# Optimization experiments

Measured on AMD Instinct MI355X. Metric: run time of the kernel, lower is better.

Reference implementation:

```python
import jax, jax.numpy as jnp
import numpy as np

N = 50000   # nodes
E = 800000  # edges
D = 200     # h_dim == out_dim
R = 500     # num_rels
L = 2       # num_hidden_layers
RRELU_SLOPE = (1.0 / 8.0 + 1.0 / 3.0) / 2.0  # eval-mode F.rrelu negative slope


def _rrelu(x):
    return jnp.where(x >= 0, x, x * jnp.float32(RRELU_SLOPE))


def setup_inputs() -> dict:
    key = jax.random.key(0)
    ks = jax.random.split(key, 10)
    s = np.float32(1.0 / np.sqrt(D))  # ~xavier scale
    return {
        "init_ent_emb": jax.random.normal(ks[0], (N, D), jnp.float32),
        "rel_emb": jax.random.normal(ks[1], (R, D), jnp.float32),
        "weight_neighbor": jax.random.normal(ks[2], (L, D, D), jnp.float32) * s,
        "loop_weight": jax.random.normal(ks[3], (L, D, D), jnp.float32) * s,
        "evolve_loop_weight": jax.random.normal(ks[4], (L, D, D), jnp.float32) * s,
        "norm": jax.random.uniform(ks[5], (N, 1), jnp.float32),
        "src": jax.random.randint(ks[6], (E,), 0, N, dtype=jnp.int32),
        "dst": jax.random.randint(ks[7], (E,), 0, N, dtype=jnp.int32),
        "etype": jax.random.randint(ks[8], (E,), 0, R, dtype=jnp.int32),
        "node_id": jnp.arange(N, dtype=jnp.int32),
    }


def reference(init_ent_emb, rel_emb, weight_neighbor, loop_weight,
              evolve_loop_weight, norm, src, dst, etype, node_id):
    # g.ndata['h'] = init_ent_emb[node_id]
    h = init_ent_emb[node_id]                                    # [N, D]
    # mask of nodes with in-degree > 0 (fixed across layers)
    indeg = jnp.zeros((N,), jnp.float32).at[dst].add(1.0)
    has_in = (indeg > 0)[:, None]                                # [N, 1]
    for l in range(L):
        # loop message: loop_weight where in-degree>0, evolve_loop_weight otherwise
        loop_msg = jnp.where(has_in,
                             h @ loop_weight[l],
                             h @ evolve_loop_weight[l])          # [N, D]
        # per-edge message: (h_src + rel_emb[etype]) @ W_neighbor
        msg = (h[src] + rel_emb[etype]) @ weight_neighbor[l]     # [E, D]
        # sum-scatter to destination nodes, then per-node norm (apply_func)
        agg = jax.ops.segment_sum(msg, dst, num_segments=N)      # [N, D]
        h = _rrelu(agg * norm + loop_msg)
    return h
```

## Files before the change

### kernel.cpp

```cpp
#include <hip/hip_runtime.h>

#define D 200
#define RRELU_SLOPE 0.22916666666666666f
#define STRIDE 96
#define PAD 8

typedef unsigned short u16;
typedef unsigned int u32;

using bf16x8 = __attribute__((ext_vector_type(8))) short;
using f32x4  = __attribute__((ext_vector_type(4))) float;
using f32x2  = __attribute__((ext_vector_type(2))) float;

__device__ __forceinline__ float rrelu(float x) {
    return x >= 0.0f ? x : x * RRELU_SLOPE;
}
__device__ __forceinline__ float bf2f(u32 u) {
    union { u32 i; float f; } c; c.i = u << 16; return c.f;
}
__device__ __forceinline__ u32 f2bf(float f) {
    union { float f; u32 i; } c; c.f = f;
    return (c.i + 0x7fffu + ((c.i >> 16) & 1u)) >> 16;
}
__device__ __forceinline__ u32 pack2(float x, float y) {
    return f2bf(x) | (f2bf(y) << 16);
}
__device__ __forceinline__ void gll16(const void* g, void* l) {
    __builtin_amdgcn_global_load_lds((const __attribute__((address_space(1))) void*)g,
                                     (__attribute__((address_space(3))) void*)l,
                                     16, 0, 0);
}

__device__ __forceinline__ void accw(u32 w, f32x2& acc) {
    union { u32 i; float f; } lo, hi;
    lo.i = w << 16;
    hi.i = w & 0xffff0000u;
    f32x2 t; t[0] = lo.f; t[1] = hi.f;
    acc += t;
}
__device__ __forceinline__ void accq(uint4 q, f32x2* a) {
    accw(q.x, a[0]); accw(q.y, a[1]); accw(q.z, a[2]); accw(q.w, a[3]);
}


__global__ void prep_k(const float* __restrict__ rel, const float* __restrict__ Wn,
                       const float* __restrict__ Wl, u16* __restrict__ relb,
                       u16* __restrict__ Bt, u16* __restrict__ hb0d,
                       u16* __restrict__ hb1d, int* __restrict__ noin_cnt) {
    int i = blockIdx.x * blockDim.x + threadIdx.x;
    if (i == 0) *noin_cnt = 0;
    if (i < 200) { hb0d[i] = 0; hb1d[i] = 0; }
    if (i < 100200) relb[i] = (i < 100000) ? (u16)f2bf(rel[i]) : (u16)0;
    if (i < 2 * 256 * 416) {
        int l = i / (256 * 416);
        int rem = i % (256 * 416);
        int c = rem / 416;
        int k = rem % 416;
        float v = 0.0f;
        if (c < 200 && k < 400)
            v = (k < 200) ? Wn[(size_t)l * 40000 + k * 200 + c]
                          : Wl[(size_t)l * 40000 + (k - 200) * 200 + c];
        Bt[i] = (u16)f2bf(v);
    }
}


__global__ void scatter_k(const int* __restrict__ dst, const int* __restrict__ src,
                          const int* __restrict__ etype, int* __restrict__ cnt,
                          u32* __restrict__ ep, int E) {
    int e = blockIdx.x * blockDim.x + threadIdx.x;
    if (e < E) {
        int d = dst[e];
        int c = atomicAdd(&cnt[d], 1);
        if (c < STRIDE)
            ep[(size_t)d * STRIDE + c] = (u32)src[e] | ((u32)etype[e] << 17);
    }
}

__global__ void pad_k(const int* __restrict__ cnt, u32* __restrict__ ep, u32 dummy,
                      int* __restrict__ noin, int* __restrict__ noin_cnt, int N) {
    int v = blockIdx.x * blockDim.x + threadIdx.x;
    if (v >= N) return;
    int c = cnt[v];
    if (c == 0) noin[atomicAdd(noin_cnt, 1)] = v;
    int e = (c + PAD - 1) & ~(PAD - 1);
    for (int i = c; i < e; ++i) ep[(size_t)v * STRIDE + i] = dummy;
}


__global__ void gather_k(const float* __restrict__ init, const int* __restrict__ nid,
                         u16* __restrict__ hb, int N) {
    int lane = threadIdx.x & 63;
    int v = blockIdx.x * 4 + (threadIdx.x >> 6);
    if (v >= N || lane >= 50) return;
    float4 f = *(const float4*)(init + (size_t)nid[v] * D + lane * 4);
    uint2 o;
    o.x = pack2(f.x, f.y);
    o.y = pack2(f.z, f.w);
    *(uint2*)(hb + (size_t)v * D + lane * 4) = o;
}


__global__ __launch_bounds__(256) void gagg0_k(
        const u16* __restrict__ hb, const u16* __restrict__ relb,
        const u32* __restrict__ ep, const int* __restrict__ cnt,
        const float* __restrict__ norm,
        u16* __restrict__ aggb, u16* __restrict__ relsumb, int N, u32 dummy) {
    int lane = threadIdx.x & 63;
    int wave = threadIdx.x >> 6;
    int li = lane & 31;
    int v = blockIdx.x * 8 + wave * 2 + (lane >> 5);
    if (v >= N || li >= 25) return;
    size_t lo = (size_t)li * 8;
    const u16* hbL = hb + lo;
    const u16* rbL = relb + lo;
    int c = cnt[v];
    if (c > STRIDE) c = STRIDE;
    int rv = (c + PAD - 1) >> 3;
    const u32* pp = ep + (size_t)v * STRIDE;
    f32x2 a[4] = {}, rr[4] = {};
    u32 p[8];
    uint4 qh[8];
#pragma unroll
    for (int j = 0; j < 8; ++j) p[j] = (rv > 0) ? pp[j] : dummy;
#pragma unroll
    for (int j = 0; j < 8; ++j)
        qh[j] = *(const uint4*)(hbL + (size_t)(p[j] & 0x1FFFFu) * D);
    for (int r = 0; r < rv; ++r) {
        u32 pn[8];
#pragma unroll
        for (int j = 0; j < 8; ++j)
            pn[j] = (r + 1 < rv) ? pp[(size_t)(r + 1) * 8 + j] : dummy;
        uint4 qr[8];
#pragma unroll
        for (int j = 0; j < 8; ++j)
            qr[j] = *(const uint4*)(rbL + (size_t)((p[j] >> 17) & 0x3FFu) * D);
#pragma unroll
        for (int j = 0; j < 8; ++j) accq(qh[j], a);
#pragma unroll
        for (int j = 0; j < 8; ++j)
            qh[j] = *(const uint4*)(hbL + (size_t)(pn[j] & 0x1FFFFu) * D);
#pragma unroll
        for (int j = 0; j < 8; ++j) accq(qr[j], rr);
#pragma unroll
        for (int j = 0; j < 8; ++j) p[j] = pn[j];
    }
    uint4 rs;
    rs.x = pack2(rr[0][0], rr[0][1]); rs.y = pack2(rr[1][0], rr[1][1]);
    rs.z = pack2(rr[2][0], rr[2][1]); rs.w = pack2(rr[3][0], rr[3][1]);
    *(uint4*)(relsumb + (size_t)v * D + lo) = rs;
    float nv = norm[v];
    uint4 o;
    o.x = pack2((a[0][0] + rr[0][0]) * nv, (a[0][1] + rr[0][1]) * nv);
    o.y = pack2((a[1][0] + rr[1][0]) * nv, (a[1][1] + rr[1][1]) * nv);
    o.z = pack2((a[2][0] + rr[2][0]) * nv, (a[2][1] + rr[2][1]) * nv);
    o.w = pack2((a[3][0] + rr[3][0]) * nv, (a[3][1] + rr[3][1]) * nv);
    *(uint4*)(aggb + (size_t)v * D + lo) = o;
}


__global__ __launch_bounds__(256) void gagg1_k(
        const u16* __restrict__ hb, const u32* __restrict__ ep,
        const int* __restrict__ cnt, const float* __restrict__ norm,
        const u16* __restrict__ addb, u16* __restrict__ outb, int N, u32 dummy) {
    int lane = threadIdx.x & 63;
    int wave = threadIdx.x >> 6;
    int li = lane & 31;
    int v = blockIdx.x * 8 + wave * 2 + (lane >> 5);
    if (v >= N || li >= 25) return;
    size_t lo = (size_t)li * 8;
    const u16* hbL = hb + lo;
    int c = cnt[v];
    if (c > STRIDE) c = STRIDE;
    int rv = (c + PAD - 1) >> 3;
    const u32* pp = ep + (size_t)v * STRIDE;
    f32x2 a[4] = {};
    u32 p[8];
    uint4 qh[8];
#pragma unroll
    for (int j = 0; j < 8; ++j) p[j] = (rv > 0) ? pp[j] : dummy;
#pragma unroll
    for (int j = 0; j < 8; ++j)
        qh[j] = *(const uint4*)(hbL + (size_t)(p[j] & 0x1FFFFu) * D);
    for (int r = 0; r < rv; ++r) {
        u32 pn[8];
#pragma unroll
        for (int j = 0; j < 8; ++j)
            pn[j] = (r + 1 < rv) ? pp[(size_t)(r + 1) * 8 + j] : dummy;
#pragma unroll
        for (int j = 0; j < 8; ++j) accq(qh[j], a);
#pragma unroll
        for (int j = 0; j < 8; ++j)
            qh[j] = *(const uint4*)(hbL + (size_t)(pn[j] & 0x1FFFFu) * D);
#pragma unroll
        for (int j = 0; j < 8; ++j) p[j] = pn[j];
    }
    {
        uint4 q = *(const uint4*)(addb + (size_t)v * D + lo);
        accq(q, a);
    }
    float nv = norm[v];
    uint4 o;
    o.x = pack2(a[0][0] * nv, a[0][1] * nv);
    o.y = pack2(a[1][0] * nv, a[1][1] * nv);
    o.z = pack2(a[2][0] * nv, a[2][1] * nv);
    o.w = pack2(a[3][0] * nv, a[3][1] * nv);
    *(uint4*)(outb + (size_t)v * D + lo) = o;
}


__global__ __launch_bounds__(256) void gemm_k(
        const u16* __restrict__ Aagg, const u16* __restrict__ Ah,
        const u16* __restrict__ Bt,
        float* __restrict__ outF, u16* __restrict__ outB, int M) {
    __shared__ __align__(16) u16 As[128 * 32];
    __shared__ __align__(16) u16 Bs[64 * 32];
    int tid = threadIdx.x;
    int lane = tid & 63;
    int wave = tid >> 6;
    int rowBase = blockIdx.x * 128;
    int colBase = blockIdx.y * 64;
    int wr = (wave >> 1) * 64;
    int wc = (wave & 1) * 32;
    int m = lane & 15;
    int kq = (lane >> 4) * 8;

    int srow = tid >> 2;
    int kg = (tid & 3) * 8;

    u16* ldsA0 = As + ((size_t)(wave * 64) * 8);
    u16* ldsA1 = As + ((size_t)(256 + wave * 64) * 8);
    u16* ldsB  = Bs + ((size_t)(wave * 64) * 8);

    f32x4 acc[4][2] = {};

    for (int k0 = 0; k0 < 416; k0 += 32) {
        int k = k0 + kg;
        {
            const u16* g0 = (k < 200) ? Aagg + (size_t)(rowBase + srow) * D + k
                                      : Ah + (size_t)(rowBase + srow) * D + (k - 200);
            gll16(g0, ldsA0);
            const u16* g1 = (k < 200) ? Aagg + (size_t)(rowBase + srow + 64) * D + k
                                      : Ah + (size_t)(rowBase + srow + 64) * D + (k - 200);
            gll16(g1, ldsA1);
            const u16* gb = Bt + (size_t)(colBase + srow) * 416 + k;
            gll16(gb, ldsB);
        }
        __syncthreads();

        bf16x8 a0 = *(const bf16x8*)(As + (wr + m) * 32 + kq);
        bf16x8 a1 = *(const bf16x8*)(As + (wr + 16 + m) * 32 + kq);
        bf16x8 a2 = *(const bf16x8*)(As + (wr + 32 + m) * 32 + kq);
        bf16x8 a3 = *(const bf16x8*)(As + (wr + 48 + m) * 32 + kq);
        bf16x8 b0 = *(const bf16x8*)(Bs + (wc + m) * 32 + kq);
        bf16x8 b1 = *(const bf16x8*)(Bs + (wc + 16 + m) * 32 + kq);
        acc[0][0] = __builtin_amdgcn_mfma_f32_16x16x32_bf16(a0, b0, acc[0][0], 0, 0, 0);
        acc[0][1] = __builtin_amdgcn_mfma_f32_16x16x32_bf16(a0, b1, acc[0][1], 0, 0, 0);
        acc[1][0] = __builtin_amdgcn_mfma_f32_16x16x32_bf16(a1, b0, acc[1][0], 0, 0, 0);
        acc[1][1] = __builtin_amdgcn_mfma_f32_16x16x32_bf16(a1, b1, acc[1][1], 0, 0, 0);
        acc[2][0] = __builtin_amdgcn_mfma_f32_16x16x32_bf16(a2, b0, acc[2][0], 0, 0, 0);
        acc[2][1] = __builtin_amdgcn_mfma_f32_16x16x32_bf16(a2, b1, acc[2][1], 0, 0, 0);
        acc[3][0] = __builtin_amdgcn_mfma_f32_16x16x32_bf16(a3, b0, acc[3][0], 0, 0, 0);
        acc[3][1] = __builtin_amdgcn_mfma_f32_16x16x32_bf16(a3, b1, acc[3][1], 0, 0, 0);
        __syncthreads();
    }

    int cRow = (lane >> 4) * 4;
    int cCol = lane & 15;
#pragma unroll
    for (int i = 0; i < 4; ++i) {
#pragma unroll
        for (int j = 0; j < 2; ++j) {
            int col = colBase + wc + j * 16 + cCol;
            if (col >= 200) continue;
#pragma unroll
            for (int r = 0; r < 4; ++r) {
                int row = rowBase + wr + i * 16 + cRow + r;
                if (row < M) {
                    float val = rrelu(acc[i][j][r]);
                    if (outF) outF[(size_t)row * D + col] = val;
                    if (outB) outB[(size_t)row * D + col] = (u16)f2bf(val);
                }
            }
        }
    }
}


__global__ void fixup_k(const u16* __restrict__ hb, const float* __restrict__ We,
                        const int* __restrict__ noin, const int* __restrict__ noin_cnt,
                        float* __restrict__ outF, u16* __restrict__ outB) {
    int cnt = *noin_cnt;
    for (int i = blockIdx.x; i < cnt; i += gridDim.x) {
        int v = noin[i];
        int j = threadIdx.x;
        if (j < D) {
            float acc = 0.0f;
            for (int k = 0; k < D; ++k)
                acc += bf2f(hb[(size_t)v * D + k]) * We[(size_t)k * D + j];
            float r = rrelu(acc);
            if (outF) outF[(size_t)v * D + j] = r;
            if (outB) outB[(size_t)v * D + j] = (u16)f2bf(r);
        }
    }
}

extern "C" void kernel_launch(void* const* d_in, const int* in_sizes, int n_in,
                              void* d_out, int out_size, void* d_ws, size_t ws_size,
                              hipStream_t stream) {
    const float* init  = (const float*)d_in[0];
    const float* rel   = (const float*)d_in[1];
    const float* Wn    = (const float*)d_in[2];
    const float* Wl    = (const float*)d_in[3];
    const float* We    = (const float*)d_in[4];
    const float* norm  = (const float*)d_in[5];
    const int* src     = (const int*)d_in[6];
    const int* dst     = (const int*)d_in[7];
    const int* etype   = (const int*)d_in[8];
    const int* node_id = (const int*)d_in[9];
    float* out = (float*)d_out;

    int N = in_sizes[5];
    int E = in_sizes[6];
    size_t NP = (size_t)N + 256;

    char* w = (char*)d_ws;
    auto carve = [&](size_t bytes) {
        char* p = w;
        w += (bytes + 255) & ~(size_t)255;
        return p;
    };
    u16* hb0     = (u16*)carve(NP * D * sizeof(u16));
    u16* hb1     = (u16*)carve(NP * D * sizeof(u16));
    u16* aggb    = (u16*)carve(NP * D * sizeof(u16));
    u16* relsumb = (u16*)carve((size_t)N * D * sizeof(u16));
    u16* relb    = (u16*)carve((size_t)501 * D * sizeof(u16));
    u16* Bt      = (u16*)carve((size_t)2 * 256 * 416 * sizeof(u16));
    int* cnt     = (int*)carve((size_t)N * sizeof(int));
    u32* epack   = (u32*)carve(((size_t)N * STRIDE + PAD) * sizeof(u32));
    int* noin    = (int*)carve((size_t)N * sizeof(int));
    int* noin_cnt = (int*)carve(sizeof(int));

    (void)hipMemsetAsync(cnt, 0, (size_t)N * sizeof(int), stream);

    int prepN = 2 * 256 * 416;
    prep_k<<<(prepN + 255) / 256, 256, 0, stream>>>(rel, Wn, Wl, relb, Bt,
                                                    hb0 + (size_t)N * D,
                                                    hb1 + (size_t)N * D, noin_cnt);
    scatter_k<<<(E + 255) / 256, 256, 0, stream>>>(dst, src, etype, cnt, epack, E);
    u32 dummy = (u32)N | (500u << 17);
    pad_k<<<(N + 255) / 256, 256, 0, stream>>>(cnt, epack, dummy, noin, noin_cnt, N);
    gather_k<<<(N + 3) / 4, 256, 0, stream>>>(init, node_id, hb0, N);

    dim3 gg((N + 127) / 128, 4);

    gagg0_k<<<(N + 7) / 8, 256, 0, stream>>>(hb0, relb, epack, cnt, norm,
                                             aggb, relsumb, N, dummy);
    gemm_k<<<gg, 256, 0, stream>>>(aggb, hb0, Bt, nullptr, hb1, N);
    fixup_k<<<8, 256, 0, stream>>>(hb0, We, noin, noin_cnt, nullptr, hb1);

    gagg1_k<<<(N + 7) / 8, 256, 0, stream>>>(hb1, epack, cnt, norm,
                                             relsumb, aggb, N, dummy);
    gemm_k<<<gg, 256, 0, stream>>>(aggb, hb1, Bt + 256 * 416, out, nullptr, N);
    fixup_k<<<8, 256, 0, stream>>>(hb1, We + D * D, noin, noin_cnt, out, nullptr);
}
```

Measured before the change: 376.5 us.

## Retile GEMM to 64-row blocks covering all output columns per block

The fused aggregation+loop GEMM now assigns each block 64 rows and all 256 padded output columns, with each wave computing a 64x64 tile, instead of a 128x64 tile over a 2D grid. The A rows (agg and h) are then read from global memory once instead of once per column block, which cuts redundant activation traffic. In exchange each block loads the full weight slice every k-step, needs more LDS and twice the accumulator registers, and the last column tile still computes padded columns past 200.

```diff
diff --git a/kernel.cpp b/kernel.cpp
--- a/kernel.cpp
+++ b/kernel.cpp
@@ -213,55 +213,61 @@
         const u16* __restrict__ Aagg, const u16* __restrict__ Ah,
         const u16* __restrict__ Bt,
         float* __restrict__ outF, u16* __restrict__ outB, int M) {
-    __shared__ __align__(16) u16 As[128 * 32];
-    __shared__ __align__(16) u16 Bs[64 * 32];
+    __shared__ __align__(16) u16 As[64 * 32];
+    __shared__ __align__(16) u16 Bs[256 * 32];
     int tid = threadIdx.x;
     int lane = tid & 63;
     int wave = tid >> 6;
-    int rowBase = blockIdx.x * 128;
-    int colBase = blockIdx.y * 64;
-    int wr = (wave >> 1) * 64;
-    int wc = (wave & 1) * 32;
+    int rowBase = blockIdx.x * 64;
     int m = lane & 15;
     int kq = (lane >> 4) * 8;
 
     int srow = tid >> 2;
     int kg = (tid & 3) * 8;
 
-    u16* ldsA0 = As + ((size_t)(wave * 64) * 8);
-    u16* ldsA1 = As + ((size_t)(256 + wave * 64) * 8);
-    u16* ldsB  = Bs + ((size_t)(wave * 64) * 8);
-
-    f32x4 acc[4][2] = {};
+    u16* ldsA = As + (size_t)wave * 512;
+
+    f32x4 acc[4][4] = {};
 
     for (int k0 = 0; k0 < 416; k0 += 32) {
         int k = k0 + kg;
         {
-            const u16* g0 = (k < 200) ? Aagg + (size_t)(rowBase + srow) * D + k
+            const u16* gA = (k < 200) ? Aagg + (size_t)(rowBase + srow) * D + k
                                       : Ah + (size_t)(rowBase + srow) * D + (k - 200);
-            gll16(g0, ldsA0);
-            const u16* g1 = (k < 200) ? Aagg + (size_t)(rowBase + srow + 64) * D + k
-                                      : Ah + (size_t)(rowBase + srow + 64) * D + (k - 200);
-            gll16(g1, ldsA1);
-            const u16* gb = Bt + (size_t)(colBase + srow) * 416 + k;
-            gll16(gb, ldsB);
+            gll16(gA, ldsA);
+#pragma unroll
+            for (int p = 0; p < 4; ++p) {
+                const u16* gB = Bt + (size_t)(p * 64 + srow) * 416 + k;
+                gll16(gB, Bs + ((size_t)p * 2048 + wave * 512));
+            }
         }
         __syncthreads();
 
-        bf16x8 a0 = *(const bf16x8*)(As + (wr + m) * 32 + kq);
-        bf16x8 a1 = *(const bf16x8*)(As + (wr + 16 + m) * 32 + kq);
-        bf16x8 a2 = *(const bf16x8*)(As + (wr + 32 + m) * 32 + kq);
-        bf16x8 a3 = *(const bf16x8*)(As + (wr + 48 + m) * 32 + kq);
+        bf16x8 a0 = *(const bf16x8*)(As + (m) * 32 + kq);
+        bf16x8 a1 = *(const bf16x8*)(As + (16 + m) * 32 + kq);
+        bf16x8 a2 = *(const bf16x8*)(As + (32 + m) * 32 + kq);
+        bf16x8 a3 = *(const bf16x8*)(As + (48 + m) * 32 + kq);
+        int wc = wave * 64;
         bf16x8 b0 = *(const bf16x8*)(Bs + (wc + m) * 32 + kq);
         bf16x8 b1 = *(const bf16x8*)(Bs + (wc + 16 + m) * 32 + kq);
+        bf16x8 b2 = *(const bf16x8*)(Bs + (wc + 32 + m) * 32 + kq);
+        bf16x8 b3 = *(const bf16x8*)(Bs + (wc + 48 + m) * 32 + kq);
         acc[0][0] = __builtin_amdgcn_mfma_f32_16x16x32_bf16(a0, b0, acc[0][0], 0, 0, 0);
         acc[0][1] = __builtin_amdgcn_mfma_f32_16x16x32_bf16(a0, b1, acc[0][1], 0, 0, 0);
+        acc[0][2] = __builtin_amdgcn_mfma_f32_16x16x32_bf16(a0, b2, acc[0][2], 0, 0, 0);
+        acc[0][3] = __builtin_amdgcn_mfma_f32_16x16x32_bf16(a0, b3, acc[0][3], 0, 0, 0);
         acc[1][0] = __builtin_amdgcn_mfma_f32_16x16x32_bf16(a1, b0, acc[1][0], 0, 0, 0);
         acc[1][1] = __builtin_amdgcn_mfma_f32_16x16x32_bf16(a1, b1, acc[1][1], 0, 0, 0);
+        acc[1][2] = __builtin_amdgcn_mfma_f32_16x16x32_bf16(a1, b2, acc[1][2], 0, 0, 0);
+        acc[1][3] = __builtin_amdgcn_mfma_f32_16x16x32_bf16(a1, b3, acc[1][3], 0, 0, 0);
         acc[2][0] = __builtin_amdgcn_mfma_f32_16x16x32_bf16(a2, b0, acc[2][0], 0, 0, 0);
         acc[2][1] = __builtin_amdgcn_mfma_f32_16x16x32_bf16(a2, b1, acc[2][1], 0, 0, 0);
+        acc[2][2] = __builtin_amdgcn_mfma_f32_16x16x32_bf16(a2, b2, acc[2][2], 0, 0, 0);
+        acc[2][3] = __builtin_amdgcn_mfma_f32_16x16x32_bf16(a2, b3, acc[2][3], 0, 0, 0);
         acc[3][0] = __builtin_amdgcn_mfma_f32_16x16x32_bf16(a3, b0, acc[3][0], 0, 0, 0);
         acc[3][1] = __builtin_amdgcn_mfma_f32_16x16x32_bf16(a3, b1, acc[3][1], 0, 0, 0);
+        acc[3][2] = __builtin_amdgcn_mfma_f32_16x16x32_bf16(a3, b2, acc[3][2], 0, 0, 0);
+        acc[3][3] = __builtin_amdgcn_mfma_f32_16x16x32_bf16(a3, b3, acc[3][3], 0, 0, 0);
         __syncthreads();
     }
 
@@ -270,12 +276,12 @@
 #pragma unroll
     for (int i = 0; i < 4; ++i) {
 #pragma unroll
-        for (int j = 0; j < 2; ++j) {
-            int col = colBase + wc + j * 16 + cCol;
+        for (int j = 0; j < 4; ++j) {
+            int col = wave * 64 + j * 16 + cCol;
             if (col >= 200) continue;
 #pragma unroll
             for (int r = 0; r < 4; ++r) {
-                int row = rowBase + wr + i * 16 + cRow + r;
+                int row = rowBase + i * 16 + cRow + r;
                 if (row < M) {
                     float val = rrelu(acc[i][j][r]);
                     if (outF) outF[(size_t)row * D + col] = val;
@@ -352,15 +358,15 @@
     pad_k<<<(N + 255) / 256, 256, 0, stream>>>(cnt, epack, dummy, noin, noin_cnt, N);
     gather_k<<<(N + 3) / 4, 256, 0, stream>>>(init, node_id, hb0, N);
 
-    dim3 gg((N + 127) / 128, 4);
+    int gemmBlocks = (N + 63) / 64;
 
     gagg0_k<<<(N + 7) / 8, 256, 0, stream>>>(hb0, relb, epack, cnt, norm,
                                              aggb, relsumb, N, dummy);
-    gemm_k<<<gg, 256, 0, stream>>>(aggb, hb0, Bt, nullptr, hb1, N);
+    gemm_k<<<gemmBlocks, 256, 0, stream>>>(aggb, hb0, Bt, nullptr, hb1, N);
     fixup_k<<<8, 256, 0, stream>>>(hb0, We, noin, noin_cnt, nullptr, hb1);
 
     gagg1_k<<<(N + 7) / 8, 256, 0, stream>>>(hb1, epack, cnt, norm,
                                              relsumb, aggb, N, dummy);
-    gemm_k<<<gg, 256, 0, stream>>>(aggb, hb1, Bt + 256 * 416, out, nullptr, N);
+    gemm_k<<<gemmBlocks, 256, 0, stream>>>(aggb, hb1, Bt + 256 * 416, out, nullptr, N);
     fixup_k<<<8, 256, 0, stream>>>(hb1, We + D * D, noin, noin_cnt, out, nullptr);
 }
```

Measured after the change: 358.0 us. -4.9%, faster.
